# Kernel tuning notes

Measured on AMD Instinct MI355X. Metric: run time of the kernel, lower is better.

## Reference

```python
import jax, jax.numpy as jnp
import numpy as np

EPS_BN = 1e-5
EPS_LN = 1e-5
EPS_L2 = 1e-12


def adder2d(x, w, stride):
    """AdderNet pseudo-conv: out = -sum |x_patch - w| (negative L1 distance).
    x: (N, Cin, H, W); w: (Cout, Cin, kh, kw); no padding, no bias.
    Loops only over the small fixed kernel footprint (<=12 positions) to avoid
    materializing the full im2col L1 tensor at once.
    """
    N, Cin, H, W = x.shape
    Cout, _, kh, kw = w.shape
    sh, sw = stride
    Ho = (H - kh) // sh + 1
    Wo = (W - kw) // sw + 1
    out = jnp.zeros((N, Ho, Wo, Cout), dtype=x.dtype)
    for i in range(kh):
        for j in range(kw):
            # strided slice of the input for this kernel tap: (N, Cin, Ho, Wo)
            xs = x[:, :, i:i + sh * Ho:sh, j:j + sw * Wo:sw]
            xs = jnp.transpose(xs, (0, 2, 3, 1))          # (N, Ho, Wo, Cin)
            wt = w[:, :, i, j]                            # (Cout, Cin)
            # |x - w| summed over Cin -> (N, Ho, Wo, Cout)
            out = out - jnp.abs(xs[:, :, :, None, :] - wt[None, None, None, :, :]).sum(-1)
    return jnp.transpose(out, (0, 3, 1, 2))               # (N, Cout, Ho, Wo)


def bn_relu(x, gamma, beta):
    # training-mode BatchNorm2d (batch statistics, biased var) + ReLU
    mean = x.mean(axis=(0, 2, 3), keepdims=True)
    var = x.var(axis=(0, 2, 3), keepdims=True)
    y = (x - mean) * jax.lax.rsqrt(var + EPS_BN)
    y = y * gamma[None, :, None, None] + beta[None, :, None, None]
    return jax.nn.relu(y)


def setup_inputs() -> dict:
    key = jax.random.key(0)
    ks = jax.random.split(key, 8)
    N = 16
    x = jax.random.normal(ks[0], (N, 1, 196, 3), dtype=jnp.float32)
    w1 = jax.random.normal(ks[1], (128, 1, 6, 1), dtype=jnp.float32) * 0.1
    w2 = jax.random.normal(ks[2], (256, 128, 6, 1), dtype=jnp.float32) * 0.05
    w3 = jax.random.normal(ks[3], (384, 256, 6, 2), dtype=jnp.float32) * 0.05
    g1, b1 = jnp.ones((128,), jnp.float32), jnp.zeros((128,), jnp.float32)
    g2, b2 = jnp.ones((256,), jnp.float32), jnp.zeros((256,), jnp.float32)
    g3, b3 = jnp.ones((384,), jnp.float32), jnp.zeros((384,), jnp.float32)
    Wfc = jax.random.normal(ks[4], (6, 16128), dtype=jnp.float32) * (1.0 / np.sqrt(16128))
    bfc = jax.random.normal(ks[5], (6,), dtype=jnp.float32) * 0.01
    return {"x": x, "w1": w1, "g1": g1, "b1": b1, "w2": w2, "g2": g2, "b2": b2,
            "w3": w3, "g3": g3, "b3": b3, "Wfc": Wfc, "bfc": bfc}


def reference(x, w1, g1, b1, w2, g2, b2, w3, g3, b3, Wfc, bfc):
    h = bn_relu(adder2d(x, w1, (2, 1)), g1, b1)   # (N,128,96,3)
    h = bn_relu(adder2d(h, w2, (2, 1)), g2, b2)   # (N,256,46,3)
    h = bn_relu(adder2d(h, w3, (2, 1)), g3, b3)   # (N,384,21,2)
    h = h.reshape(h.shape[0], -1)                  # (N,16128)
    h = h @ Wfc.T + bfc                            # (N,6)
    # nn.LayerNorm(x.size()) normalizes over ALL dims (batch included), weight=1 bias=0
    mu = h.mean()
    var = h.var()
    h = (h - mu) * jax.lax.rsqrt(var + EPS_LN)
    # F.normalize: per-row L2 normalization
    norm = jnp.sqrt((h * h).sum(axis=1, keepdims=True))
    return h / jnp.maximum(norm, EPS_L2)
```

## Files before the change

kernel.cpp:

```cpp
#include <hip/hip_runtime.h>
#include <math.h>

#define DEVINL __device__ __forceinline__

DEVINL float absadd(float a, float b) {
  float t;
  asm("v_add_f32 %0, |%1|, |%2|" : "=v"(t) : "v"(a), "v"(b));
  return t;
}

template<int NWAVES>
DEVINL void block_reduce_2d(double& a, double& b) {
  #pragma unroll
  for (int off = 32; off > 0; off >>= 1) {
    a += __shfl_down(a, off, 64);
    b += __shfl_down(b, off, 64);
  }
  __shared__ double sa[NWAVES], sb[NWAVES];
  const int tid = threadIdx.x;
  const int wid = tid >> 6;
  if ((tid & 63) == 0) { sa[wid] = a; sb[wid] = b; }
  __syncthreads();
  if (tid == 0) {
    double ta = 0.0, tb = 0.0;
    #pragma unroll
    for (int w = 0; w < NWAVES; ++w) { ta += sa[w]; tb += sb[w]; }
    a = ta; b = tb;
  }
}

__global__ __launch_bounds__(256) void k_conv1(
    const float* __restrict__ x, const float* __restrict__ w1,
    const float* __restrict__ g1, const float* __restrict__ b1,
    float* __restrict__ h1) {
  __shared__ float xlds[9408];
  const int co = blockIdx.x;
  const int tid = threadIdx.x;
  {
    float4* xd = (float4*)xlds;
    const float4* xs = (const float4*)x;
    #pragma unroll
    for (int k = 0; k < 10; ++k) {
      const int f = tid + k * 256;
      if (f < 2352) xd[f] = xs[f];
    }
  }
  float wv[6];
  #pragma unroll
  for (int i = 0; i < 6; ++i) wv[i] = w1[co * 6 + i];
  __syncthreads();

  float vals[18];
  double s = 0.0, sq = 0.0;
  #pragma unroll
  for (int k = 0; k < 18; ++k) {
    const int p = tid + k * 256;
    const int n = p / 288;
    const int r = p - n * 288;
    const int ho = r / 3;
    const int wo = r - ho * 3;
    const float* xb = xlds + n * 588 + (2 * ho) * 3 + wo;
    float e0 = xb[0]  - wv[0];
    float e1 = xb[3]  - wv[1];
    float e2 = xb[6]  - wv[2];
    float e3 = xb[9]  - wv[3];
    float e4 = xb[12] - wv[4];
    float e5 = xb[15] - wv[5];
    const float t0 = absadd(e0, e1);
    const float t1 = absadd(e2, e3);
    const float t2 = absadd(e4, e5);
    const float v = -((t0 + t1) + t2);
    vals[k] = v;
    s += (double)v;
    sq += (double)v * (double)v;
  }
  block_reduce_2d<4>(s, sq);
  __shared__ float ssc, ssh;
  if (tid == 0) {
    const double mean = s * (1.0 / 4608.0);
    const double var  = sq * (1.0 / 4608.0) - mean * mean;
    const float rstd = (float)rsqrt(var + 1e-5);
    const float sc = g1[co] * rstd;
    ssc = sc;
    ssh = b1[co] - (float)mean * sc;
  }
  __syncthreads();
  const float sc = ssc, sh = ssh;
  #pragma unroll
  for (int k = 0; k < 18; ++k) {
    const int p = tid + k * 256;
    const int n = p / 288;
    const int r = p - n * 288;
    const int ho = r / 3;
    const int wo = r - ho * 3;
    h1[((n * 128 + co) * 96 + ho) * 3 + wo] = fmaxf(0.f, fmaf(vals[k], sc, sh));
  }
}

__global__ __launch_bounds__(192) void k_conv2p(
    const float* __restrict__ h1, const float* __restrict__ w2,
    float* __restrict__ part2) {
  __shared__ float wlds[512];
  __shared__ float4 xbuf[2][584];
  const int bx = blockIdx.x;
  const int kc = bx & 7;
  const int rbx = bx >> 3;
  const int cg = rbx & 63;
  const int nh = rbx >> 6;
  const int co0 = cg * 4, ci0 = kc * 16, n0 = nh * 8;
  const int tid = threadIdx.x;
  #pragma unroll
  for (int f = tid; f < 512; f += 192) {
    const int cil = f >> 5, rem = f & 31, c = rem >> 3, kk = rem & 7;
    wlds[f] = (kk < 6) ? w2[(co0 + c) * 768 + (ci0 + cil) * 6 + kk] : 0.f;
  }
  const bool active = tid < 184;
  const int n = tid / 23, hp = tid - n * 23;

  int s_lds[3], s_g[3];
  #pragma unroll
  for (int k = 0; k < 3; ++k) {
    const int f = tid + k * 192;
    const int nn = f / 72, j = f - nn * 72;
    s_lds[k] = nn * 73 + j;
    s_g[k]   = (n0 + nn) * 9216 + j;
  }
  const float4* h1v = (const float4*)h1;

  float acc[4][6];
  #pragma unroll
  for (int c = 0; c < 4; ++c)
    #pragma unroll
    for (int o = 0; o < 6; ++o) acc[c][o] = 0.f;

  float4 r[3];
  #pragma unroll
  for (int k = 0; k < 3; ++k) r[k] = h1v[s_g[k] + ci0 * 72];
  #pragma unroll
  for (int k = 0; k < 3; ++k) xbuf[0][s_lds[k]] = r[k];
  #pragma unroll
  for (int k = 0; k < 3; ++k) r[k] = h1v[s_g[k] + (ci0 + 1) * 72];
  __syncthreads();

  const float4* wl4 = (const float4*)wlds;
  #pragma unroll 1
  for (int ci = 0; ci < 16; ++ci) {
    const float4* cur = xbuf[ci & 1];
    if (ci + 1 < 16) {
      float4* nxt = xbuf[(ci + 1) & 1];
      #pragma unroll
      for (int k = 0; k < 3; ++k) nxt[s_lds[k]] = r[k];
    }
    if (ci + 2 < 16) {
      #pragma unroll
      for (int k = 0; k < 3; ++k) r[k] = h1v[s_g[k] + (ci0 + ci + 2) * 72];
    }
    if (active) {
      const float4* xr = cur + n * 73 + hp * 3;
      float xf[24];
      #pragma unroll
      for (int t = 0; t < 6; ++t) {
        const float4 q = xr[t];
        xf[4 * t + 0] = q.x; xf[4 * t + 1] = q.y; xf[4 * t + 2] = q.z; xf[4 * t + 3] = q.w;
      }
      #pragma unroll
      for (int c = 0; c < 4; ++c) {
        const float4 wa = wl4[(ci * 4 + c) * 2];
        const float4 wb = wl4[(ci * 4 + c) * 2 + 1];
        const float wv[6] = {wa.x, wa.y, wa.z, wa.w, wb.x, wb.y};
        #pragma unroll
        for (int po = 0; po < 2; ++po)
          #pragma unroll
          for (int wo = 0; wo < 3; ++wo) {
            float e0 = xf[(2 * po + 0) * 3 + wo] - wv[0];
            float e1 = xf[(2 * po + 1) * 3 + wo] - wv[1];
            float e2 = xf[(2 * po + 2) * 3 + wo] - wv[2];
            float e3 = xf[(2 * po + 3) * 3 + wo] - wv[3];
            float e4 = xf[(2 * po + 4) * 3 + wo] - wv[4];
            float e5 = xf[(2 * po + 5) * 3 + wo] - wv[5];
            const float t0 = absadd(e0, e1);
            const float t1 = absadd(e2, e3);
            const float t2 = absadd(e4, e5);
            acc[c][po * 3 + wo] += (t0 + t1) + t2;
          }
      }
    }
    __syncthreads();
  }
  if (active) {
    #pragma unroll
    for (int c = 0; c < 4; ++c)
      #pragma unroll
      for (int po = 0; po < 2; ++po)
        #pragma unroll
        for (int wo = 0; wo < 3; ++wo) {
          const int p = (n0 + n) * 138 + (2 * hp + po) * 3 + wo;
          part2[(size_t)(kc * 256 + co0 + c) * 2208 + p] = acc[c][po * 3 + wo];
        }
  }
}

__global__ __launch_bounds__(384) void k_combine2(
    const float* __restrict__ part2, const float* __restrict__ g2,
    const float* __restrict__ b2, float* __restrict__ h2) {
  const int co = blockIdx.x;
  const int tid = threadIdx.x;
  const bool active = tid < 368;
  float v[6];
  double s = 0.0, sq = 0.0;
  #pragma unroll
  for (int k = 0; k < 6; ++k) {
    float sum = 0.f;
    if (active) {
      const int p = tid + k * 368;
      #pragma unroll
      for (int kc = 0; kc < 8; ++kc)
        sum += part2[(size_t)(kc * 256 + co) * 2208 + p];
    }
    const float val = -sum;
    v[k] = val;
    if (active) { s += (double)val; sq += (double)val * (double)val; }
  }
  block_reduce_2d<6>(s, sq);
  __shared__ float ssc, ssh;
  if (tid == 0) {
    const double mean = s * (1.0 / 2208.0);
    const double var  = sq * (1.0 / 2208.0) - mean * mean;
    const float rstd = (float)rsqrt(var + 1e-5);
    const float sc = g2[co] * rstd;
    ssc = sc;
    ssh = b2[co] - (float)mean * sc;
  }
  __syncthreads();
  if (active) {
    const float sc = ssc, sh = ssh;
    #pragma unroll
    for (int k = 0; k < 6; ++k) {
      const int p = tid + k * 368;
      const int n = p / 138, rem = p - n * 138;
      h2[n * 35328 + co * 138 + rem] = fmaxf(0.f, fmaf(v[k], sc, sh));
    }
  }
}

__global__ __launch_bounds__(128) void k_conv3p(
    const float* __restrict__ h2, const float* __restrict__ w3,
    float* __restrict__ part3) {
  __shared__ float wlds[768];
  __shared__ float2 xbuf[2][284];
  const int bx = blockIdx.x;
  const int kc = bx & 15;
  const int rbx = bx >> 4;
  const int cg = rbx % 96;
  const int nh = rbx / 96;
  const int co0 = cg * 4, ci0 = kc * 16, n0 = nh * 4;
  const int tid = threadIdx.x;
  #pragma unroll
  for (int f = tid; f < 768; f += 128) {
    const int cil = f / 48, rem = f - cil * 48, c = rem / 12, kk = rem - c * 12;
    wlds[f] = w3[(co0 + c) * 3072 + (ci0 + cil) * 12 + kk];
  }
  const bool active = tid < 112;
  const int n = tid / 28;
  const int rem28 = tid - n * 28;
  const int hot = rem28 >> 2;
  const int cq = rem28 & 3;

  int s_lds[3], s_g[3];
  const bool v3 = tid < 20;
  #pragma unroll
  for (int k = 0; k < 3; ++k) {
    const int f = tid + k * 128;
    const int nn = f / 69, j = f - nn * 69;
    s_lds[k] = nn * 71 + j;
    s_g[k]   = (n0 + nn) * 17664 + j;
  }
  const float2* h2v = (const float2*)h2;

  float acc[3][2];
  #pragma unroll
  for (int h = 0; h < 3; ++h) { acc[h][0] = 0.f; acc[h][1] = 0.f; }

  float2 r[3];
  #pragma unroll
  for (int k = 0; k < 2; ++k) r[k] = h2v[s_g[k] + ci0 * 69];
  if (v3) r[2] = h2v[s_g[2] + ci0 * 69];
  #pragma unroll
  for (int k = 0; k < 2; ++k) xbuf[0][s_lds[k]] = r[k];
  if (v3) xbuf[0][s_lds[2]] = r[2];
  #pragma unroll
  for (int k = 0; k < 2; ++k) r[k] = h2v[s_g[k] + (ci0 + 1) * 69];
  if (v3) r[2] = h2v[s_g[2] + (ci0 + 1) * 69];
  __syncthreads();

  const float4* wl4 = (const float4*)wlds;
  #pragma unroll 1
  for (int ci = 0; ci < 16; ++ci) {
    const float2* cur = xbuf[ci & 1];
    if (ci + 1 < 16) {
      float2* nxt = xbuf[(ci + 1) & 1];
      #pragma unroll
      for (int k = 0; k < 2; ++k) nxt[s_lds[k]] = r[k];
      if (v3) nxt[s_lds[2]] = r[2];
    }
    if (ci + 2 < 16) {
      #pragma unroll
      for (int k = 0; k < 2; ++k) r[k] = h2v[s_g[k] + (ci0 + ci + 2) * 69];
      if (v3) r[2] = h2v[s_g[2] + (ci0 + ci + 2) * 69];
    }
    if (active) {
      float xf[30];
      const float2* xr = cur + n * 71 + 9 * hot;
      #pragma unroll
      for (int t = 0; t < 15; ++t) {
        const float2 q = xr[t];
        xf[2 * t + 0] = q.x; xf[2 * t + 1] = q.y;
      }
      const float4 w0 = wl4[(ci * 4 + cq) * 3];
      const float4 w1 = wl4[(ci * 4 + cq) * 3 + 1];
      const float4 w2q = wl4[(ci * 4 + cq) * 3 + 2];
      const float wv[12] = {w0.x, w0.y, w0.z, w0.w, w1.x, w1.y,
                            w1.z, w1.w, w2q.x, w2q.y, w2q.z, w2q.w};
      #pragma unroll
      for (int h = 0; h < 3; ++h)
        #pragma unroll
        for (int wo = 0; wo < 2; ++wo) {
          float e0  = xf[(2 * h + 0) * 3 + wo]     - wv[0];
          float e1  = xf[(2 * h + 0) * 3 + wo + 1] - wv[1];
          float e2  = xf[(2 * h + 1) * 3 + wo]     - wv[2];
          float e3  = xf[(2 * h + 1) * 3 + wo + 1] - wv[3];
          float e4  = xf[(2 * h + 2) * 3 + wo]     - wv[4];
          float e5  = xf[(2 * h + 2) * 3 + wo + 1] - wv[5];
          float e6  = xf[(2 * h + 3) * 3 + wo]     - wv[6];
          float e7  = xf[(2 * h + 3) * 3 + wo + 1] - wv[7];
          float e8  = xf[(2 * h + 4) * 3 + wo]     - wv[8];
          float e9  = xf[(2 * h + 4) * 3 + wo + 1] - wv[9];
          float e10 = xf[(2 * h + 5) * 3 + wo]     - wv[10];
          float e11 = xf[(2 * h + 5) * 3 + wo + 1] - wv[11];
          const float t0 = absadd(e0, e1);
          const float t1 = absadd(e2, e3);
          const float t2 = absadd(e4, e5);
          const float t3 = absadd(e6, e7);
          const float t4 = absadd(e8, e9);
          const float t5 = absadd(e10, e11);
          acc[h][wo] += ((t0 + t1) + (t2 + t3)) + (t4 + t5);
        }
    }
    __syncthreads();
  }
  if (active) {
    #pragma unroll
    for (int h = 0; h < 3; ++h) {
      const int ho = 3 * hot + h;
      #pragma unroll
      for (int wo = 0; wo < 2; ++wo) {
        const int p = (n0 + n) * 42 + ho * 2 + wo;
        part3[(size_t)(kc * 384 + co0 + cq) * 672 + p] = acc[h][wo];
      }
    }
  }
}

__global__ __launch_bounds__(384) void k_combine3(
    const float* __restrict__ part3, const float* __restrict__ g3,
    const float* __restrict__ b3, float* __restrict__ h3) {
  const int co = blockIdx.x;
  const int tid = threadIdx.x;
  const bool active = tid < 336;
  float v[2];
  double s = 0.0, sq = 0.0;
  #pragma unroll
  for (int k = 0; k < 2; ++k) {
    float sum = 0.f;
    if (active) {
      const int p = tid + k * 336;
      #pragma unroll
      for (int kc = 0; kc < 16; ++kc)
        sum += part3[(size_t)(kc * 384 + co) * 672 + p];
    }
    const float val = -sum;
    v[k] = val;
    if (active) { s += (double)val; sq += (double)val * (double)val; }
  }
  block_reduce_2d<6>(s, sq);
  __shared__ float ssc, ssh;
  if (tid == 0) {
    const double mean = s * (1.0 / 672.0);
    const double var  = sq * (1.0 / 672.0) - mean * mean;
    const float rstd = (float)rsqrt(var + 1e-5);
    const float sc = g3[co] * rstd;
    ssc = sc;
    ssh = b3[co] - (float)mean * sc;
  }
  __syncthreads();
  if (active) {
    const float sc = ssc, sh = ssh;
    #pragma unroll
    for (int k = 0; k < 2; ++k) {
      const int p = tid + k * 336;
      const int n = p / 42, rem = p - n * 42;
      h3[n * 16128 + co * 42 + rem] = fmaxf(0.f, fmaf(v[k], sc, sh));
    }
  }
}

__global__ __launch_bounds__(256) void k_fcp(
    const float* __restrict__ h3, const float* __restrict__ Wfc,
    float* __restrict__ hfcp) {
  const int bx = blockIdx.x;
  const int pair = bx >> 2, q = bx & 3;
  const int n = pair / 6, o = pair - n * 6;
  const float4* xr = (const float4*)(h3 + n * 16128) + q * 1008;
  const float4* wr = (const float4*)(Wfc + o * 16128) + q * 1008;
  float sacc = 0.f;
  for (int k = threadIdx.x; k < 1008; k += 256) {
    const float4 xv = xr[k];
    const float4 wv = wr[k];
    sacc += xv.x * wv.x + xv.y * wv.y + xv.z * wv.z + xv.w * wv.w;
  }
  double d = (double)sacc, dummy = 0.0;
  block_reduce_2d<4>(d, dummy);
  if (threadIdx.x == 0) hfcp[bx] = (float)d;
}

__global__ __launch_bounds__(128) void k_final(
    const float* __restrict__ hfcp, const float* __restrict__ bfc,
    float* __restrict__ out) {
  __shared__ float ys[96];
  __shared__ float params[2];
  const int tid = threadIdx.x;
  float v = 0.f;
  if (tid < 96) {
    v = hfcp[tid * 4 + 0] + hfcp[tid * 4 + 1] + hfcp[tid * 4 + 2] + hfcp[tid * 4 + 3]
        + bfc[tid % 6];
    ys[tid] = v;
  }
  __syncthreads();
  if (tid == 0) {
    double s = 0.0, sq = 0.0;
    for (int i = 0; i < 96; ++i) { const double t = (double)ys[i]; s += t; sq += t * t; }
    const double mu = s / 96.0;
    const double var = sq / 96.0 - mu * mu;
    params[0] = (float)mu;
    params[1] = (float)rsqrt(var + 1e-5);
  }
  __syncthreads();
  const float y = (v - params[0]) * params[1];
  __syncthreads();
  if (tid < 96) ys[tid] = y;
  __syncthreads();
  if (tid < 96) {
    const int n = tid / 6;
    float ss = 0.f;
    #pragma unroll
    for (int k = 0; k < 6; ++k) { const float t = ys[n * 6 + k]; ss += t * t; }
    const float norm = sqrtf(ss);
    out[tid] = y / fmaxf(norm, 1e-12f);
  }
}

extern "C" void kernel_launch(void* const* d_in, const int* in_sizes, int n_in,
                              void* d_out, int out_size, void* d_ws, size_t ws_size,
                              hipStream_t stream) {
  const float* x   = (const float*)d_in[0];
  const float* w1  = (const float*)d_in[1];
  const float* g1  = (const float*)d_in[2];
  const float* b1  = (const float*)d_in[3];
  const float* w2  = (const float*)d_in[4];
  const float* g2  = (const float*)d_in[5];
  const float* b2  = (const float*)d_in[6];
  const float* w3  = (const float*)d_in[7];
  const float* g3  = (const float*)d_in[8];
  const float* b3  = (const float*)d_in[9];
  const float* Wfc = (const float*)d_in[10];
  const float* bfc = (const float*)d_in[11];

  float* ws   = (float*)d_ws;
  float* h1   = ws;
  float* h2   = h1 + 589824;
  float* h3   = h2 + 565248;
  float* hfcp = h3 + 258048;
  float* part = hfcp + 384;
  float* out  = (float*)d_out;

  k_conv1   <<<128, 256, 0, stream>>>(x, w1, g1, b1, h1);
  k_conv2p  <<<1024, 192, 0, stream>>>(h1, w2, part);
  k_combine2<<<256, 384, 0, stream>>>(part, g2, b2, h2);
  k_conv3p  <<<6144, 128, 0, stream>>>(h2, w3, part);
  k_combine3<<<384, 384, 0, stream>>>(part, g3, b3, h3);
  k_fcp     <<<384, 256, 0, stream>>>(h3, Wfc, hfcp);
  k_final   <<<1, 128, 0, stream>>>(hfcp, bfc, out);
}
```

Measured before the change: 127.2 us.

## Compute four output channels per thread in conv3 and cover full batch per block

The conv3 partial kernel now has each thread accumulate all four output channels of its channel group instead of one. Each block now covers all 16 batch items rather than a quarter of them, so the grid shrinks by four. Each staged input row and set of loaded x values is reused across four weight sets, cutting redundant LDS and global loads and block overheads. In exchange it needs more registers and LDS per block, and fewer blocks means less parallelism and latency hiding per channel slice.

```diff
diff --git a/kernel.cpp b/kernel.cpp
--- a/kernel.cpp
+++ b/kernel.cpp
@@ -247,13 +247,10 @@
     const float* __restrict__ h2, const float* __restrict__ w3,
     float* __restrict__ part3) {
   __shared__ float wlds[768];
-  __shared__ float2 xbuf[2][284];
+  __shared__ float2 xbuf[2][1136];
   const int bx = blockIdx.x;
-  const int kc = bx & 15;
-  const int rbx = bx >> 4;
-  const int cg = rbx % 96;
-  const int nh = rbx / 96;
-  const int co0 = cg * 4, ci0 = kc * 16, n0 = nh * 4;
+  const int cg = bx >> 4, kc = bx & 15;
+  const int co0 = cg * 4, ci0 = kc * 16;
   const int tid = threadIdx.x;
   #pragma unroll
   for (int f = tid; f < 768; f += 128) {
@@ -261,36 +258,35 @@
     wlds[f] = w3[(co0 + c) * 3072 + (ci0 + cil) * 12 + kk];
   }
   const bool active = tid < 112;
-  const int n = tid / 28;
-  const int rem28 = tid - n * 28;
-  const int hot = rem28 >> 2;
-  const int cq = rem28 & 3;
-
-  int s_lds[3], s_g[3];
-  const bool v3 = tid < 20;
-  #pragma unroll
-  for (int k = 0; k < 3; ++k) {
+  const int n = tid / 7, hot = tid - n * 7;
+
+  int s_lds[9], s_g[9];
+  const bool v9 = tid < 80;
+  #pragma unroll
+  for (int k = 0; k < 9; ++k) {
     const int f = tid + k * 128;
     const int nn = f / 69, j = f - nn * 69;
     s_lds[k] = nn * 71 + j;
-    s_g[k]   = (n0 + nn) * 17664 + j;
+    s_g[k]   = nn * 17664 + j;
   }
   const float2* h2v = (const float2*)h2;
 
-  float acc[3][2];
-  #pragma unroll
-  for (int h = 0; h < 3; ++h) { acc[h][0] = 0.f; acc[h][1] = 0.f; }
-
-  float2 r[3];
-  #pragma unroll
-  for (int k = 0; k < 2; ++k) r[k] = h2v[s_g[k] + ci0 * 69];
-  if (v3) r[2] = h2v[s_g[2] + ci0 * 69];
-  #pragma unroll
-  for (int k = 0; k < 2; ++k) xbuf[0][s_lds[k]] = r[k];
-  if (v3) xbuf[0][s_lds[2]] = r[2];
-  #pragma unroll
-  for (int k = 0; k < 2; ++k) r[k] = h2v[s_g[k] + (ci0 + 1) * 69];
-  if (v3) r[2] = h2v[s_g[2] + (ci0 + 1) * 69];
+  float acc[4][3][2];
+  #pragma unroll
+  for (int c = 0; c < 4; ++c)
+    #pragma unroll
+    for (int h = 0; h < 3; ++h) { acc[c][h][0] = 0.f; acc[c][h][1] = 0.f; }
+
+  float2 r[9];
+  #pragma unroll
+  for (int k = 0; k < 8; ++k) r[k] = h2v[s_g[k] + ci0 * 69];
+  if (v9) r[8] = h2v[s_g[8] + ci0 * 69];
+  #pragma unroll
+  for (int k = 0; k < 8; ++k) xbuf[0][s_lds[k]] = r[k];
+  if (v9) xbuf[0][s_lds[8]] = r[8];
+  #pragma unroll
+  for (int k = 0; k < 8; ++k) r[k] = h2v[s_g[k] + (ci0 + 1) * 69];
+  if (v9) r[8] = h2v[s_g[8] + (ci0 + 1) * 69];
   __syncthreads();
 
   const float4* wl4 = (const float4*)wlds;
@@ -300,13 +296,13 @@
     if (ci + 1 < 16) {
       float2* nxt = xbuf[(ci + 1) & 1];
       #pragma unroll
-      for (int k = 0; k < 2; ++k) nxt[s_lds[k]] = r[k];
-      if (v3) nxt[s_lds[2]] = r[2];
+      for (int k = 0; k < 8; ++k) nxt[s_lds[k]] = r[k];
+      if (v9) nxt[s_lds[8]] = r[8];
     }
     if (ci + 2 < 16) {
       #pragma unroll
-      for (int k = 0; k < 2; ++k) r[k] = h2v[s_g[k] + (ci0 + ci + 2) * 69];
-      if (v3) r[2] = h2v[s_g[2] + (ci0 + ci + 2) * 69];
+      for (int k = 0; k < 8; ++k) r[k] = h2v[s_g[k] + (ci0 + ci + 2) * 69];
+      if (v9) r[8] = h2v[s_g[8] + (ci0 + ci + 2) * 69];
     }
     if (active) {
       float xf[30];
@@ -316,48 +312,53 @@
         const float2 q = xr[t];
         xf[2 * t + 0] = q.x; xf[2 * t + 1] = q.y;
       }
-      const float4 w0 = wl4[(ci * 4 + cq) * 3];
-      const float4 w1 = wl4[(ci * 4 + cq) * 3 + 1];
-      const float4 w2q = wl4[(ci * 4 + cq) * 3 + 2];
-      const float wv[12] = {w0.x, w0.y, w0.z, w0.w, w1.x, w1.y,
-                            w1.z, w1.w, w2q.x, w2q.y, w2q.z, w2q.w};
-      #pragma unroll
-      for (int h = 0; h < 3; ++h)
+      #pragma unroll
+      for (int c = 0; c < 4; ++c) {
+        const float4 w0 = wl4[(ci * 4 + c) * 3];
+        const float4 w1 = wl4[(ci * 4 + c) * 3 + 1];
+        const float4 w2q = wl4[(ci * 4 + c) * 3 + 2];
+        const float wv[12] = {w0.x, w0.y, w0.z, w0.w, w1.x, w1.y,
+                              w1.z, w1.w, w2q.x, w2q.y, w2q.z, w2q.w};
+        #pragma unroll
+        for (int h = 0; h < 3; ++h)
+          #pragma unroll
+          for (int wo = 0; wo < 2; ++wo) {
+            float e0  = xf[(2 * h + 0) * 3 + wo]     - wv[0];
+            float e1  = xf[(2 * h + 0) * 3 + wo + 1] - wv[1];
+            float e2  = xf[(2 * h + 1) * 3 + wo]     - wv[2];
+            float e3  = xf[(2 * h + 1) * 3 + wo + 1] - wv[3];
+            float e4  = xf[(2 * h + 2) * 3 + wo]     - wv[4];
+            float e5  = xf[(2 * h + 2) * 3 + wo + 1] - wv[5];
+            float e6  = xf[(2 * h + 3) * 3 + wo]     - wv[6];
+            float e7  = xf[(2 * h + 3) * 3 + wo + 1] - wv[7];
+            float e8  = xf[(2 * h + 4) * 3 + wo]     - wv[8];
+            float e9  = xf[(2 * h + 4) * 3 + wo + 1] - wv[9];
+            float e10 = xf[(2 * h + 5) * 3 + wo]     - wv[10];
+            float e11 = xf[(2 * h + 5) * 3 + wo + 1] - wv[11];
+            const float t0 = absadd(e0, e1);
+            const float t1 = absadd(e2, e3);
+            const float t2 = absadd(e4, e5);
+            const float t3 = absadd(e6, e7);
+            const float t4 = absadd(e8, e9);
+            const float t5 = absadd(e10, e11);
+            acc[c][h][wo] += ((t0 + t1) + (t2 + t3)) + (t4 + t5);
+          }
+      }
+    }
+    __syncthreads();
+  }
+  if (active) {
+    #pragma unroll
+    for (int c = 0; c < 4; ++c)
+      #pragma unroll
+      for (int h = 0; h < 3; ++h) {
+        const int ho = 3 * hot + h;
         #pragma unroll
         for (int wo = 0; wo < 2; ++wo) {
-          float e0  = xf[(2 * h + 0) * 3 + wo]     - wv[0];
-          float e1  = xf[(2 * h + 0) * 3 + wo + 1] - wv[1];
-          float e2  = xf[(2 * h + 1) * 3 + wo]     - wv[2];
-          float e3  = xf[(2 * h + 1) * 3 + wo + 1] - wv[3];
-          float e4  = xf[(2 * h + 2) * 3 + wo]     - wv[4];
-          float e5  = xf[(2 * h + 2) * 3 + wo + 1] - wv[5];
-          float e6  = xf[(2 * h + 3) * 3 + wo]     - wv[6];
-          float e7  = xf[(2 * h + 3) * 3 + wo + 1] - wv[7];
-          float e8  = xf[(2 * h + 4) * 3 + wo]     - wv[8];
-          float e9  = xf[(2 * h + 4) * 3 + wo + 1] - wv[9];
-          float e10 = xf[(2 * h + 5) * 3 + wo]     - wv[10];
-          float e11 = xf[(2 * h + 5) * 3 + wo + 1] - wv[11];
-          const float t0 = absadd(e0, e1);
-          const float t1 = absadd(e2, e3);
-          const float t2 = absadd(e4, e5);
-          const float t3 = absadd(e6, e7);
-          const float t4 = absadd(e8, e9);
-          const float t5 = absadd(e10, e11);
-          acc[h][wo] += ((t0 + t1) + (t2 + t3)) + (t4 + t5);
+          const int p = n * 42 + ho * 2 + wo;
+          part3[(size_t)(kc * 384 + co0 + c) * 672 + p] = acc[c][h][wo];
         }
-    }
-    __syncthreads();
-  }
-  if (active) {
-    #pragma unroll
-    for (int h = 0; h < 3; ++h) {
-      const int ho = 3 * hot + h;
-      #pragma unroll
-      for (int wo = 0; wo < 2; ++wo) {
-        const int p = (n0 + n) * 42 + ho * 2 + wo;
-        part3[(size_t)(kc * 384 + co0 + cq) * 672 + p] = acc[h][wo];
       }
-    }
   }
 }
 
@@ -486,7 +487,7 @@
   k_conv1   <<<128, 256, 0, stream>>>(x, w1, g1, b1, h1);
   k_conv2p  <<<1024, 192, 0, stream>>>(h1, w2, part);
   k_combine2<<<256, 384, 0, stream>>>(part, g2, b2, h2);
-  k_conv3p  <<<6144, 128, 0, stream>>>(h2, w3, part);
+  k_conv3p  <<<1536, 128, 0, stream>>>(h2, w3, part);
   k_combine3<<<384, 384, 0, stream>>>(part, g3, b3, h3);
   k_fcp     <<<384, 256, 0, stream>>>(h3, Wfc, hfcp);
   k_final   <<<1, 128, 0, stream>>>(hfcp, bfc, out);
```

Measured after the change: 132.3 us. 4.0% more time.
